# Kernel optimization log

Hardware: AMD Instinct MI355X
Metric: run time of the kernel (lower is better)

Reference implementation:

```python
import jax, jax.numpy as jnp
import numpy as np

FAR = 10.0
RAST = 256          # rast_size default
ORIG_W, ORIG_H = 256.0, 256.0  # orig_size default
CHUNK = 32          # faces processed per scan step
EPS = 1e-9


def _project(vertices, K, R, t, dist):
    # persp projection with lens distortion; vertices [B,V,3] -> [B,V,3] (u,v in [-1,1], z depth)
    v = jnp.einsum('bvj,bij->bvi', vertices, R) + t
    x, y, z = v[..., 0], v[..., 1], v[..., 2]
    x_ = x / (z + EPS)
    y_ = y / (z + EPS)
    k1, k2, p1, p2, k3 = (dist[:, None, i] for i in range(5))
    r2 = x_ * x_ + y_ * y_  # == r**2 in original (r = sqrt(x_^2+y_^2))
    radial = 1.0 + k1 * r2 + k2 * r2 ** 2 + k3 * r2 ** 3
    x__ = x_ * radial + 2.0 * p1 * x_ * y_ + p2 * (r2 + 2.0 * x_ ** 2)
    y__ = y_ * radial + p1 * (r2 + 2.0 * y_ ** 2) + 2.0 * p2 * x_ * y_
    pts = jnp.stack([x__, y__, jnp.ones_like(z)], axis=-1)
    pts = jnp.einsum('bvj,bij->bvi', pts, K)
    u, vv = pts[..., 0], pts[..., 1]
    vv = ORIG_H - vv
    u = 2.0 * (u - ORIG_W / 2.0) / ORIG_W
    vv = 2.0 * (vv - ORIG_H / 2.0) / ORIG_H
    return jnp.stack([u, vv, z], axis=-1)


def _rasterize(fverts):
    # fverts: [B,F,3,3] per-face screen-space vertices (u,v,z). Z-buffer depth raster + coverage mask.
    B, F = fverts.shape[0], fverts.shape[1]
    pad = (-F) % CHUNK
    fv = jnp.pad(fverts, ((0, 0), (0, pad), (0, 0), (0, 0)))  # padded faces are degenerate (den==0)
    nc = (F + pad) // CHUNK
    fv = fv.reshape(B, nc, CHUNK, 3, 3).transpose(1, 0, 2, 3, 4)  # [nc,B,CHUNK,3,3]
    # pixel centers in [-1,1]; row i top-to-bottom maps to y = -1..1 (consistent with flipped v)
    g = 2.0 * (jnp.arange(RAST, dtype=jnp.float32) + 0.5) / RAST - 1.0
    X = g[None, None, None, :]   # cols
    Y = g[None, None, :, None]   # rows

    def body(carry, ch):
        zbuf, cover = carry
        e = lambda i, j: ch[:, :, i, j][:, :, None, None]
        ax, ay, az = e(0, 0), e(0, 1), e(0, 2)
        bx, by, bz = e(1, 0), e(1, 1), e(1, 2)
        cx, cy, cz = e(2, 0), e(2, 1), e(2, 2)
        den = (bx - ax) * (cy - ay) - (by - ay) * (cx - ax)
        ok = jnp.abs(den) > 1e-8
        den_s = jnp.where(ok, den, 1.0)
        # barycentric coords of each pixel wrt this face (signed; fill_back provides both windings)
        w0 = ((by - cy) * (X - cx) + (cx - bx) * (Y - cy)) / den_s
        w1 = ((cy - ay) * (X - cx) + (ax - cx) * (Y - cy)) / den_s
        w2 = 1.0 - w0 - w1
        zs = lambda zz: jnp.where(zz > 1e-8, zz, 1.0)
        inv = w0 / zs(az) + w1 / zs(bz) + w2 / zs(cz)  # perspective-correct 1/z interp
        valid = ok & (w0 >= 0) & (w1 >= 0) & (w2 >= 0)
        valid = valid & (az > 1e-8) & (bz > 1e-8) & (cz > 1e-8) & (inv > 1e-8)
        zp = 1.0 / jnp.where(valid, inv, 1.0)
        zc = jnp.min(jnp.where(valid, zp, FAR), axis=1)  # nearest face in this chunk [B,S,S]
        return (jnp.minimum(zbuf, zc), cover | jnp.any(valid, axis=1)), None

    zbuf0 = jnp.full((B, RAST, RAST), FAR, dtype=jnp.float32)
    cov0 = jnp.zeros((B, RAST, RAST), dtype=bool)
    (zbuf, cover), _ = jax.lax.scan(body, (zbuf0, cov0), fv)
    return zbuf, cover


def _normalize_depth(img, far):
    img_inf = (img == far).astype(jnp.float32)
    img_no_back = (1.0 - img_inf) * img
    img_max = img_no_back.max(axis=1, keepdims=True).max(axis=2, keepdims=True)
    img_min = img.min(axis=1, keepdims=True).min(axis=2, keepdims=True)
    nd = (img_max - img) / (img_max - img_min + 1e-4)
    return jnp.clip(nd, 0.0, 1.0)


def _forward(vertices, faces, intr, R, t, dist_coeffs):
    # fill_back=True: append faces with reversed vertex order
    faces_fb = jnp.concatenate([faces, faces[:, :, ::-1]], axis=1)
    uvz = _project(vertices, intr, R, t, dist_coeffs)
    fverts = jax.vmap(lambda v, f: v[f])(uvz, faces_fb)  # [B,F,3,3]
    zbuf, cover = _rasterize(fverts)
    dep = _normalize_depth(zbuf, FAR)
    mask = cover.astype(jnp.float32)
    return dep, mask


def setup_inputs():
    key = jax.random.key(0)
    k0, k1, k2 = jax.random.split(key, 3)
    B, V, F = 4, 778, 1538  # MANO hand mesh
    vertices = jax.random.normal(k0, (B, V, 3), dtype=jnp.float32) * 0.1 \
        + jnp.array([0.0, 0.0, 0.6], dtype=jnp.float32)  # blob 0.6m in front of camera
    faces = jax.random.randint(k1, (B, F, 3), 0, V, dtype=jnp.int32)
    K = jnp.tile(jnp.array([[500.0, 0.0, 128.0],
                            [0.0, 500.0, 128.0],
                            [0.0, 0.0, 1.0]], dtype=jnp.float32)[None], (B, 1, 1))
    R = jnp.tile(jnp.eye(3, dtype=jnp.float32)[None], (B, 1, 1))
    t = jnp.zeros((B, 1, 3), dtype=jnp.float32)
    dist_coeffs = jax.random.uniform(k2, (B, 5), dtype=jnp.float32) * 0.01
    return {"vertices": vertices, "faces": faces, "intr": K, "R": R, "t": t,
            "dist_coeffs": dist_coeffs}


def reference(vertices, faces, intr, R, t, dist_coeffs):
    return _forward(vertices, faces, intr, R, t, dist_coeffs)
```

## Files before the change

kernel.cpp:

```cpp
#include <hip/hip_runtime.h>
#include <cstdint>

#define RASTN 256
#define FARV 10.0f
#define FARBITS 0x41200000u
#define SPLIT 4
#define NBUCK 1024
#define NINITY 8

__device__ __forceinline__ float gval(int i) {
    return (2.0f * ((float)i + 0.5f)) / 256.0f - 1.0f;
}

__global__ __launch_bounds__(1024) void prep_sort_kernel(
    const float* __restrict__ verts, const int* __restrict__ faces,
    const float* __restrict__ Km, const float* __restrict__ Rm,
    const float* __restrict__ tm, const float* __restrict__ dm,
    float4* __restrict__ rec, uint2* __restrict__ sax, unsigned short* __restrict__ stri,
    unsigned int* __restrict__ zbits, unsigned int* __restrict__ mm,
    float* __restrict__ uvzg, int V, int F, int F2, int B, int npix)
{
#pragma clang fp contract(off)
    __shared__ float s_uvz[1024*3];
    __shared__ unsigned int s_pk[4096];
    __shared__ unsigned short s_bk[4096];
    __shared__ unsigned int s_hist[NBUCK], s_cnt2[NBUCK];
    int b = blockIdx.x, y = blockIdx.y, tid = threadIdx.x;
    uint4* zb4 = (uint4*)(zbits + (size_t)b * npix);
    int n4 = npix >> 2;
    int sl0 = (n4 * y) / NINITY, sl1 = (n4 * (y + 1)) / NINITY;
    for (int i = sl0 + tid; i < sl1; i += 1024)
        zb4[i] = make_uint4(FARBITS, FARBITS, FARBITS, FARBITS);
    if (y > 0) return;
    if (tid == 0) { mm[2*b] = 0u; mm[2*b+1] = FARBITS; }
    for (int i = tid; i < NBUCK; i += 1024) s_hist[i] = 0u;
    bool inlds = (V <= 1024);
    const float* R = Rm + b*9; const float* K = Km + b*9;
    const float* t = tm + b*3; const float* d = dm + b*5;
    for (int v = tid; v < V; v += 1024) {
        float vx = verts[((size_t)b*V + v)*3+0];
        float vy = verts[((size_t)b*V + v)*3+1];
        float vz = verts[((size_t)b*V + v)*3+2];
        float cxm = ((vx*R[0] + vy*R[1]) + vz*R[2]) + t[0];
        float cym = ((vx*R[3] + vy*R[4]) + vz*R[5]) + t[1];
        float czm = ((vx*R[6] + vy*R[7]) + vz*R[8]) + t[2];
        float zd = czm + 1e-9f;
        float x_ = cxm / zd;
        float y_ = cym / zd;
        float k1 = d[0], k2 = d[1], p1 = d[2], p2 = d[3], k3 = d[4];
        float r2   = (x_*x_) + (y_*y_);
        float r2_2 = r2 * r2;
        float r2_3 = r2 * r2_2;
        float radial = ((1.0f + k1*r2) + k2*r2_2) + k3*r2_3;
        float x__ = ((x_*radial) + (((2.0f*p1)*x_)*y_)) + (p2*(r2 + 2.0f*(x_*x_)));
        float y__ = ((y_*radial) + (p1*(r2 + 2.0f*(y_*y_)))) + (((2.0f*p2)*x_)*y_);
        float up = ((x__*K[0]) + (y__*K[1])) + (1.0f*K[2]);
        float vp = ((x__*K[3]) + (y__*K[4])) + (1.0f*K[5]);
        vp = 256.0f - vp;
        float un = (2.0f*(up - 128.0f)) / 256.0f;
        float vn = (2.0f*(vp - 128.0f)) / 256.0f;
        if (inlds) { s_uvz[v*3+0]=un; s_uvz[v*3+1]=vn; s_uvz[v*3+2]=czm; }
        else { uvzg[((size_t)b*V+v)*3+0]=un; uvzg[((size_t)b*V+v)*3+1]=vn; uvzg[((size_t)b*V+v)*3+2]=czm; }
    }
    __syncthreads();
    const float* ub = inlds ? s_uvz : (uvzg + (size_t)b*V*3);
    const int* fb = faces + (size_t)b * F * 3;
    float4* rb = rec + (size_t)b * F2 * 4;
    bool stash = (F2 <= 4096);
    for (int j = tid; j < F2; j += 1024) {
        int i0, i1, i2;
        if (j < F) { i0 = fb[j*3+0]; i1 = fb[j*3+1]; i2 = fb[j*3+2]; }
        else { int jj = j - F; i0 = fb[jj*3+2]; i1 = fb[jj*3+1]; i2 = fb[jj*3+0]; }
        float ax = ub[i0*3+0], ay = ub[i0*3+1], az = ub[i0*3+2];
        float bx = ub[i1*3+0], by = ub[i1*3+1], bz = ub[i1*3+2];
        float cx = ub[i2*3+0], cy = ub[i2*3+1], cz = ub[i2*3+2];
        float den = (bx-ax)*(cy-ay) - (by-ay)*(cx-ax);
        bool ok = fabsf(den) > 1e-8f;
        float dens = ok ? den : 1.0f;
        bool alive = ok && (az > 1e-8f) && (bz > 1e-8f) && (cz > 1e-8f);
        float za = (az > 1e-8f) ? az : 1.0f;
        float zb = (bz > 1e-8f) ? bz : 1.0f;
        float zc = (cz > 1e-8f) ? cz : 1.0f;
        float mnx = fminf(ax, fminf(bx, cx));
        float mxx = fmaxf(ax, fmaxf(bx, cx));
        float mny = fminf(ay, fminf(by, cy));
        float mxy = fmaxf(ay, fmaxf(by, cy));
        float m = 1e-3f + 1e-6f*((fabsf(mnx)+fabsf(mxx))+(fabsf(mny)+fabsf(mxy)));
        mnx -= m; mxx += m; mny -= m; mxy += m;
        if (!(mxx >= -1.0f) || !(mnx <= 1.0f) || !(mxy >= -1.0f) || !(mny <= 1.0f)) alive = false;
        int ic0 = 1, ic1 = 0, ir0 = 1, ir1 = 0;
        float minz = 3e38f;
        if (alive) {
            float lx = fmaxf(mnx, -1.5f), hx = fminf(mxx, 1.5f);
            float ly = fmaxf(mny, -1.5f), hy = fminf(mxy, 1.5f);
            ic0 = (int)floorf((lx + 1.0f) * 128.0f - 0.5f);
            ic1 = (int)ceilf ((hx + 1.0f) * 128.0f - 0.5f);
            ir0 = (int)floorf((ly + 1.0f) * 128.0f - 0.5f);
            ir1 = (int)ceilf ((hy + 1.0f) * 128.0f - 0.5f);
            ic0 = ic0 < 0 ? 0 : ic0;  ir0 = ir0 < 0 ? 0 : ir0;
            ic1 = ic1 > 255 ? 255 : ic1;  ir1 = ir1 > 255 ? 255 : ir1;
            if (ic0 > ic1 || ir0 > ir1) { ic0 = 1; ic1 = 0; ir0 = 1; ir1 = 0; minz = 3e38f; }
            else minz = fminf(za, fminf(zb, zc)) * (1.0f - 4e-4f);
        }
        float minzv = fminf(za, fminf(zb, zc));
        float maxzv = fmaxf(za, fmaxf(zb, zc));
        float rd = __builtin_amdgcn_rcpf(dens);
        float ra, rbz, rc;
        if (minzv > 1e-2f && maxzv < 100.0f * minzv) {
            ra  = __builtin_amdgcn_rcpf(za);
            rbz = __builtin_amdgcn_rcpf(zb);
            rc  = __builtin_amdgcn_rcpf(zc);
        } else {
            ra = rbz = rc = __builtin_huge_valf();
        }
        unsigned int pack = (unsigned int)(ic0 | (ic1 << 8) | (ir0 << 16) | (ir1 << 24));
        int bk = NBUCK - 1;
        if (minz < 1e30f) {
            bk = (int)(minz * 512.0f);
            bk = bk < 0 ? 0 : (bk > NBUCK-2 ? NBUCK-2 : bk);
        }
        size_t base = (size_t)j * 4;
        rb[base+0] = make_float4(cx, cy, by - cy, cx - bx);
        rb[base+1] = make_float4(cy - ay, ax - cx, rd, ra);
        rb[base+2] = make_float4(dens, za, zb, zc);
        rb[base+3] = make_float4(__uint_as_float(pack), minz, rbz, rc);
        atomicAdd(&s_hist[bk], 1u);
        if (stash) { s_pk[j] = pack; s_bk[j] = (unsigned short)bk; }
    }
    __syncthreads();
    for (int i = tid; i < NBUCK; i += 1024) s_cnt2[i] = s_hist[i];
    __syncthreads();
    for (int st = 1; st < NBUCK; st <<= 1) {
        unsigned int v = 0;
        if (tid < NBUCK && tid >= st) v = s_cnt2[tid - st];
        __syncthreads();
        if (tid < NBUCK && tid >= st) s_cnt2[tid] += v;
        __syncthreads();
    }
    if (tid < NBUCK) s_cnt2[tid] -= s_hist[tid];
    __syncthreads();
    uint2* sxb = sax + (size_t)b * F2;
    unsigned short* stb = stri + (size_t)b * F2;
    for (int j = tid; j < F2; j += 1024) {
        unsigned int pack; int bk;
        if (stash) { pack = s_pk[j]; bk = (int)s_bk[j]; }
        else {
            float4 q3 = rb[(size_t)j*4+3];
            pack = __float_as_uint(q3.x);
            float mz = q3.y;
            bk = NBUCK - 1;
            if (mz < 1e30f) { bk = (int)(mz * 512.0f); bk = bk < 0 ? 0 : (bk > NBUCK-2 ? NBUCK-2 : bk); }
        }
        float key = (bk == NBUCK-1) ? 3e38f : (float)bk * (1.0f/512.0f);
        int pos = (int)atomicAdd(&s_cnt2[bk], 1u);
        sxb[pos] = make_uint2(pack, __float_as_uint(key));
        stb[pos] = (unsigned short)j;
    }
}

__global__ __launch_bounds__(256) void raster_kernel(
    const float4* __restrict__ rec, const uint2* __restrict__ sax,
    const unsigned short* __restrict__ stri, unsigned int* __restrict__ zbits,
    int F2)
{
#pragma clang fp contract(off)
    __shared__ float4 sh[256];
    __shared__ float s_mz[64];
    __shared__ unsigned short s_list[256];
    __shared__ int s_wk[4], s_kk[4], s_wo[4];
    __shared__ int s_tot, s_kc;
    __shared__ float s_tzmax, s_red[4];
    int zz = blockIdx.z;
    int b = zz / SPLIT, sp = zz - b*SPLIT;
    int tc = blockIdx.x, tr = blockIdx.y;
    int tid = threadIdx.x, lane = tid & 63, wv = tid >> 6;
    int tx = tid & 15, ty = tid >> 4;
    int col = tc*16 + tx, row = tr*16 + ty;
    float X = gval(col), Y = gval(row);
    int pc0 = tc*16, pc1 = pc0+15, pr0 = tr*16, pr1 = pr0+15;
    const float4* rb = rec + (size_t)b * F2 * 4;
    const uint2* sxb = sax + (size_t)b * F2;
    const unsigned short* stb = stri + (size_t)b * F2;
    size_t pix = ((size_t)b*RASTN + row)*RASTN + col;
    unsigned int* zp_g = zbits + pix;
    float zmin = FARV;
    float pushed = FARV;
    if (tid == 0) s_tzmax = FARV;
    __syncthreads();
    int nch = (F2 + 256*SPLIT - 1) / (256*SPLIT);
    for (int c = 0; c < nch; ++c) {
        int s = (c*256 + tid)*SPLIT + sp;
        bool kp = false, sv = false; unsigned int tri = 0;
        if (s < F2) {
            uint2 a = sxb[s];
            float kf = __uint_as_float(a.y);
            kp = !(kf > s_tzmax);
            if (kp) {
                int pk = (int)a.x;
                int ic0 = pk & 255, ic1 = (pk >> 8) & 255;
                int ir0 = (pk >> 16) & 255, ir1 = (pk >> 24) & 255;
                sv = (ic0 <= ic1) && (ic0 <= pc1) && (ic1 >= pc0) && (ir0 <= pr1) && (ir1 >= pr0);
                if (sv) tri = stb[s];
            }
        }
        unsigned long long bs = __ballot(sv ? 1 : 0);
        unsigned long long bk = __ballot(kp ? 1 : 0);
        int pfx = __popcll(bs & ((1ull << lane) - 1ull));
        if (lane == 0) { s_wk[wv] = __popcll(bs); s_kk[wv] = __popcll(bk); }
        __syncthreads();
        if (tid == 0) {
            int acc = 0;
            for (int q = 0; q < 4; ++q) { s_wo[q] = acc; acc += s_wk[q]; }
            s_tot = acc;
            s_kc = s_kk[0] + s_kk[1] + s_kk[2] + s_kk[3];
        }
        __syncthreads();
        if (sv) s_list[s_wo[wv] + pfx] = (unsigned short)tri;
        int kcnt = s_kc, n = s_tot;
        if (kcnt == 0) break;
        for (int g = 0; g < n; g += 64) {
            __syncthreads();
            int cnt2 = (n - g) < 64 ? (n - g) : 64;
            if (tid < cnt2*4) {
                unsigned int t4 = s_list[g + (tid >> 2)];
                float4 f = rb[(size_t)t4*4 + (tid & 3)];
                sh[tid] = f;
                if ((tid & 3) == 3) s_mz[tid >> 2] = f.y;
            }
            __syncthreads();
            {
                float zg = __uint_as_float(__hip_atomic_load(
                    zp_g, __ATOMIC_RELAXED, __HIP_MEMORY_SCOPE_AGENT));
                pushed = fminf(pushed, zg);
                zmin = fminf(zmin, zg);
            }
            for (int i = 0; i < cnt2; ++i) {
                float mz = s_mz[i];
                if (mz > zmin) continue;
                float4 q3 = sh[i*4+3];
                int pk = __float_as_int(q3.x);
                int ic0 = pk & 255, ic1 = (pk >> 8) & 255;
                int ir0 = (pk >> 16) & 255, ir1 = (pk >> 24) & 255;
                if (col < ic0 || col > ic1 || row < ir0 || row > ir1) continue;
                float4 q0 = sh[i*4+0];
                float4 q1 = sh[i*4+1];
                float xc = X - q0.x;
                float yc = Y - q0.y;
                float e0 = (q0.z*xc) + (q0.w*yc);
                float e1 = (q1.x*xc) + (q1.y*yc);
                float rd = q1.z;
                float sgn = copysignf(1.0f, rd);
                float s0 = e0*sgn, s1 = e1*sgn;
                float w0a = e0*rd, w1a = e1*rd;
                float w2a = (1.0f - w0a) - w1a;
                float epsu = 1e-4f*((1.0f + fabsf(w0a)) + fabsf(w1a));
                if (s0 > -1e-30f && s1 > -1e-30f && w2a > -epsu) {
                    float inva = ((w0a*q1.w) + (w1a*q3.z)) + (w2a*q3.w);
                    float zpa = __builtin_amdgcn_rcpf(inva);
                    bool clearly = (s0 > 0.0f) && (s1 > 0.0f) && (w2a > epsu) && (inva > 1e-6f);
                    if (!clearly || zpa < zmin*1.001f) {
                        float4 q2 = sh[i*4+2];
                        float dens = q2.x;
                        float w0 = e0 / dens;
                        float w1 = e1 / dens;
                        float w2 = (1.0f - w0) - w1;
                        float inv = ((w0 / q2.y) + (w1 / q2.z)) + (w2 / q2.w);
                        if ((w0 >= 0.0f) && (w1 >= 0.0f) && (w2 >= 0.0f) && (inv > 1e-8f)) {
                            float zp = 1.0f / inv;
                            zmin = fminf(zmin, zp);
                        }
                    }
                }
            }
            if (zmin < pushed) {
                atomicMin(zp_g, __float_as_uint(zmin));
                pushed = zmin;
            }
        }
        if (n > 0) {
            float zx = zmin;
            for (int o = 32; o; o >>= 1) zx = fmaxf(zx, __shfl_xor(zx, o));
            if (lane == 0) s_red[wv] = zx;
        }
        __syncthreads();
        if (n > 0 && tid == 0)
            s_tzmax = fminf(s_tzmax,
                fmaxf(fmaxf(s_red[0], s_red[1]), fmaxf(s_red[2], s_red[3])));
        __syncthreads();
    }
    if (zmin < pushed)
        atomicMin(zp_g, __float_as_uint(zmin));
}

__global__ __launch_bounds__(256) void minmax_kernel(
    const float* __restrict__ zbuf, float* __restrict__ mask,
    unsigned int* __restrict__ mm, int npix, int seg)
{
    __shared__ float smx[4], smn[4];
    int b = blockIdx.y;
    size_t base = (size_t)b * npix + (size_t)blockIdx.x * seg;
    const float* p = zbuf + base;
    float* mk = mask + base;
    int lane = threadIdx.x & 63, wv = threadIdx.x >> 6;
    float vmx = 0.0f, vmn = FARV;
    for (int i = threadIdx.x; i < seg; i += 256) {
        float z = p[i];
        mk[i] = (z < FARV) ? 1.0f : 0.0f;
        float nb = (z == FARV) ? 0.0f : z;
        vmx = fmaxf(vmx, nb);
        vmn = fminf(vmn, z);
    }
    for (int o = 32; o; o >>= 1) {
        vmx = fmaxf(vmx, __shfl_xor(vmx, o));
        vmn = fminf(vmn, __shfl_xor(vmn, o));
    }
    if (lane == 0) { smx[wv] = vmx; smn[wv] = vmn; }
    __syncthreads();
    if (threadIdx.x == 0) {
        float bmx = fmaxf(fmaxf(smx[0], smx[1]), fmaxf(smx[2], smx[3]));
        float bmn = fminf(fminf(smn[0], smn[1]), fminf(smn[2], smn[3]));
        atomicMax(mm + 2*b,     __float_as_uint(bmx));
        atomicMin(mm + 2*b + 1, __float_as_uint(bmn));
    }
}

__global__ __launch_bounds__(256) void final_kernel(
    float* __restrict__ zdep, const unsigned int* __restrict__ mm, int npix, int total)
{
#pragma clang fp contract(off)
    int idx = blockIdx.x*256 + threadIdx.x;
    if (idx >= total) return;
    int b = idx / npix;
    float mx = __uint_as_float(mm[2*b]);
    float mn = __uint_as_float(mm[2*b + 1]);
    float z = zdep[idx];
    float nd = (mx - z) / ((mx - mn) + 1e-4f);
    float cv = nd;
    cv = (cv < 0.0f) ? 0.0f : cv;
    cv = (cv > 1.0f) ? 1.0f : cv;
    zdep[idx] = cv;
}

extern "C" void kernel_launch(void* const* d_in, const int* in_sizes, int n_in,
                              void* d_out, int out_size, void* d_ws, size_t ws_size,
                              hipStream_t stream)
{
    const float* verts = (const float*)d_in[0];
    const int*   faces = (const int*)d_in[1];
    const float* Km    = (const float*)d_in[2];
    const float* Rm    = (const float*)d_in[3];
    const float* tm    = (const float*)d_in[4];
    const float* dm    = (const float*)d_in[5];
    float* out = (float*)d_out;

    int B  = in_sizes[2] / 9;
    int V  = in_sizes[0] / (3 * B);
    int F  = in_sizes[1] / (3 * B);
    int F2 = 2 * F;
    int npix = RASTN * RASTN;

    char* ws = (char*)d_ws;
    size_t off = 0;
    float4* rec = (float4*)(ws + off);
    off = (off + (size_t)B * F2 * 4 * sizeof(float4) + 255) & ~(size_t)255;
    uint2* sax = (uint2*)(ws + off);
    off = (off + (size_t)B * F2 * sizeof(uint2) + 255) & ~(size_t)255;
    unsigned short* stri = (unsigned short*)(ws + off);
    off = (off + (size_t)B * F2 * sizeof(unsigned short) + 255) & ~(size_t)255;
    float* uvzg = (float*)(ws + off);
    off = (off + (size_t)B * V * 3 * sizeof(float) + 255) & ~(size_t)255;
    unsigned int* mm = (unsigned int*)(ws + off);

    unsigned int* zbits = (unsigned int*)out;
    float* mask = out + (size_t)B * npix;

    dim3 pgrid(B, NINITY);
    prep_sort_kernel<<<pgrid, 1024, 0, stream>>>(
        verts, faces, Km, Rm, tm, dm, rec, sax, stri, zbits, mm, uvzg,
        V, F, F2, B, npix);
    dim3 rgrid(16, 16, B * SPLIT);
    raster_kernel<<<rgrid, 256, 0, stream>>>(rec, sax, stri, zbits, F2);
    int seg = npix / 16;
    dim3 mgrid(16, B);
    minmax_kernel<<<mgrid, 256, 0, stream>>>((float*)zbits, mask, mm, npix, seg);
    final_kernel<<<(B * npix + 255) / 256, 256, 0, stream>>>((float*)zbits, mm, npix, B * npix);
}
```

Baseline: 180.3 us.

## Fuse mask and depth min/max reduction into raster kernel via last-block tile counter

Removes the separate minmax kernel. Each raster block bumps a per-tile atomic counter after its SPLIT slice, and the last of the SPLIT blocks for a tile reads the final z values, writes the mask and reduces the per-batch min/max into mm. This saves one kernel launch and a full re-read of the z buffer, at the cost of a fence, an atomic and an extra sync at the end of every raster block. The per-tile counters are zeroed in the prep kernel.

```diff
diff --git a/kernel.cpp b/kernel.cpp
--- a/kernel.cpp
+++ b/kernel.cpp
@@ -18,7 +18,8 @@
     const float* __restrict__ tm, const float* __restrict__ dm,
     float4* __restrict__ rec, uint2* __restrict__ sax, unsigned short* __restrict__ stri,
     unsigned int* __restrict__ zbits, unsigned int* __restrict__ mm,
-    float* __restrict__ uvzg, int V, int F, int F2, int B, int npix)
+    unsigned int* __restrict__ tcnt, float* __restrict__ uvzg,
+    int V, int F, int F2, int B, int npix)
 {
 #pragma clang fp contract(off)
     __shared__ float s_uvz[1024*3];
@@ -33,6 +34,7 @@
         zb4[i] = make_uint4(FARBITS, FARBITS, FARBITS, FARBITS);
     if (y > 0) return;
     if (tid == 0) { mm[2*b] = 0u; mm[2*b+1] = FARBITS; }
+    if (tid < 256) tcnt[b*256 + tid] = 0u;
     for (int i = tid; i < NBUCK; i += 1024) s_hist[i] = 0u;
     bool inlds = (V <= 1024);
     const float* R = Rm + b*9; const float* K = Km + b*9;
@@ -161,15 +163,16 @@
 __global__ __launch_bounds__(256) void raster_kernel(
     const float4* __restrict__ rec, const uint2* __restrict__ sax,
     const unsigned short* __restrict__ stri, unsigned int* __restrict__ zbits,
-    int F2)
+    float* __restrict__ mask, unsigned int* __restrict__ mm,
+    unsigned int* __restrict__ tcnt, int F2)
 {
 #pragma clang fp contract(off)
     __shared__ float4 sh[256];
     __shared__ float s_mz[64];
     __shared__ unsigned short s_list[256];
     __shared__ int s_wk[4], s_kk[4], s_wo[4];
-    __shared__ int s_tot, s_kc;
-    __shared__ float s_tzmax, s_red[4];
+    __shared__ int s_tot, s_kc, s_last;
+    __shared__ float s_tzmax, s_red[4], s_red2[4];
     int zz = blockIdx.z;
     int b = zz / SPLIT, sp = zz - b*SPLIT;
     int tc = blockIdx.x, tr = blockIdx.y;
@@ -290,37 +293,33 @@
     }
     if (zmin < pushed)
         atomicMin(zp_g, __float_as_uint(zmin));
-}
-
-__global__ __launch_bounds__(256) void minmax_kernel(
-    const float* __restrict__ zbuf, float* __restrict__ mask,
-    unsigned int* __restrict__ mm, int npix, int seg)
-{
-    __shared__ float smx[4], smn[4];
-    int b = blockIdx.y;
-    size_t base = (size_t)b * npix + (size_t)blockIdx.x * seg;
-    const float* p = zbuf + base;
-    float* mk = mask + base;
-    int lane = threadIdx.x & 63, wv = threadIdx.x >> 6;
-    float vmx = 0.0f, vmn = FARV;
-    for (int i = threadIdx.x; i < seg; i += 256) {
-        float z = p[i];
-        mk[i] = (z < FARV) ? 1.0f : 0.0f;
+    __syncthreads();
+    if (tid == 0) {
+        __threadfence();
+        unsigned int old = __hip_atomic_fetch_add(
+            tcnt + b*256 + (tr*16 + tc), 1u, __ATOMIC_ACQ_REL, __HIP_MEMORY_SCOPE_AGENT);
+        s_last = (old == SPLIT - 1) ? 1 : 0;
+    }
+    __syncthreads();
+    if (s_last) {
+        __threadfence();
+        float z = __uint_as_float(__hip_atomic_load(
+            zp_g, __ATOMIC_RELAXED, __HIP_MEMORY_SCOPE_AGENT));
+        mask[pix] = (z < FARV) ? 1.0f : 0.0f;
         float nb = (z == FARV) ? 0.0f : z;
-        vmx = fmaxf(vmx, nb);
-        vmn = fminf(vmn, z);
-    }
-    for (int o = 32; o; o >>= 1) {
-        vmx = fmaxf(vmx, __shfl_xor(vmx, o));
-        vmn = fminf(vmn, __shfl_xor(vmn, o));
-    }
-    if (lane == 0) { smx[wv] = vmx; smn[wv] = vmn; }
-    __syncthreads();
-    if (threadIdx.x == 0) {
-        float bmx = fmaxf(fmaxf(smx[0], smx[1]), fmaxf(smx[2], smx[3]));
-        float bmn = fminf(fminf(smn[0], smn[1]), fminf(smn[2], smn[3]));
-        atomicMax(mm + 2*b,     __float_as_uint(bmx));
-        atomicMin(mm + 2*b + 1, __float_as_uint(bmn));
+        float a = nb, mn = z;
+        for (int o = 32; o; o >>= 1) {
+            a  = fmaxf(a,  __shfl_xor(a,  o));
+            mn = fminf(mn, __shfl_xor(mn, o));
+        }
+        if (lane == 0) { s_red[wv] = a; s_red2[wv] = mn; }
+        __syncthreads();
+        if (tid == 0) {
+            float bmx = fmaxf(fmaxf(s_red[0], s_red[1]), fmaxf(s_red[2], s_red[3]));
+            float bmn = fminf(fminf(s_red2[0], s_red2[1]), fminf(s_red2[2], s_red2[3]));
+            atomicMax(mm + 2*b,     __float_as_uint(bmx));
+            atomicMin(mm + 2*b + 1, __float_as_uint(bmn));
+        }
     }
 }
 
@@ -370,18 +369,17 @@
     float* uvzg = (float*)(ws + off);
     off = (off + (size_t)B * V * 3 * sizeof(float) + 255) & ~(size_t)255;
     unsigned int* mm = (unsigned int*)(ws + off);
+    off = (off + (size_t)B * 2 * sizeof(unsigned int) + 255) & ~(size_t)255;
+    unsigned int* tcnt = (unsigned int*)(ws + off);
 
     unsigned int* zbits = (unsigned int*)out;
     float* mask = out + (size_t)B * npix;
 
     dim3 pgrid(B, NINITY);
     prep_sort_kernel<<<pgrid, 1024, 0, stream>>>(
-        verts, faces, Km, Rm, tm, dm, rec, sax, stri, zbits, mm, uvzg,
+        verts, faces, Km, Rm, tm, dm, rec, sax, stri, zbits, mm, tcnt, uvzg,
         V, F, F2, B, npix);
     dim3 rgrid(16, 16, B * SPLIT);
-    raster_kernel<<<rgrid, 256, 0, stream>>>(rec, sax, stri, zbits, F2);
-    int seg = npix / 16;
-    dim3 mgrid(16, B);
-    minmax_kernel<<<mgrid, 256, 0, stream>>>((float*)zbits, mask, mm, npix, seg);
+    raster_kernel<<<rgrid, 256, 0, stream>>>(rec, sax, stri, zbits, mask, mm, tcnt, F2);
     final_kernel<<<(B * npix + 255) / 256, 256, 0, stream>>>((float*)zbits, mm, npix, B * npix);
 }
```

New measurement: 332.3 us. +84.3%, slower.
